# Kernel optimization log

Hardware: AMD Instinct MI355X
Metric: run time of the kernel (lower is better)

Reference implementation:

```python
import jax, jax.numpy as jnp
import numpy as np

B, W, N = 4, 8, 1024
F_IN, HID, OUT = 256, 256, 128


def setup_inputs() -> dict:
    key = jax.random.key(0)
    ks = jax.random.split(key, 8)
    X = jax.random.normal(ks[0], (B, W, N, F_IN), dtype=jnp.float32)
    adj = jax.random.uniform(ks[1], (B, W, N, N), dtype=jnp.float32)
    # Linear params, torch default init: U(-1/sqrt(fan_in), 1/sqrt(fan_in))
    def lin(k, fi, fo):
        k1, k2 = jax.random.split(k)
        bnd = 1.0 / np.sqrt(fi)
        Wm = jax.random.uniform(k1, (fi, fo), minval=-bnd, maxval=bnd, dtype=jnp.float32)
        bm = jax.random.uniform(k2, (fo,), minval=-bnd, maxval=bnd, dtype=jnp.float32)
        return Wm, bm
    W1, b1 = lin(ks[2], F_IN, HID)
    W2, b2 = lin(ks[3], HID, HID)
    W3, b3 = lin(ks[4], HID, OUT)
    return {"X": X, "adj": adj, "W1": W1, "b1": b1, "W2": W2, "b2": b2, "W3": W3, "b3": b3}


def _normalize(adj):
    # adj: [B, W, N, N]. adj_hat = adj + I; sym degree norm D^-1/2 A D^-1/2
    n = adj.shape[-1]
    adj_hat = adj + jnp.eye(n, dtype=adj.dtype)
    d = jnp.sum(adj_hat, axis=-1) ** (-0.5)            # [B, W, N]
    # diag(d) @ adj_hat @ diag(d) == row/col scaling (same math, no N^3 diag matmuls)
    return adj_hat * d[..., :, None] * d[..., None, :]


def reference(X, adj, W1, b1, W2, b2, W3, b3):
    adj_norm = _normalize(adj)                          # [B, W, N, N]
    h = X
    for Wm, bm in ((W1, b1), (W2, b2), (W3, b3)):
        h = jnp.einsum('bwnm,bwmf->bwnf', adj_norm, h)  # aggregate
        h = jax.nn.relu(jnp.einsum('bwnf,fo->bwno', h, Wm) + bm)
    return h                                            # [B, W, N, OUT]
```

## Files before the change

kernel.cpp:

```cpp
#include <hip/hip_runtime.h>
#include <hip/hip_bf16.h>
#include <cstdint>
#include <cstddef>

#define NN 1024
#define FF 256

typedef __attribute__((ext_vector_type(8))) short bf16x8;
typedef __attribute__((ext_vector_type(4))) float f32x4;

typedef __attribute__((address_space(1))) const void* gas_ptr;
typedef __attribute__((address_space(3))) void* las_ptr;

__device__ __forceinline__ short f2bf(float x) {
  unsigned int u = __float_as_uint(x);
  u = (u + 0x7fffu + ((u >> 16) & 1u)) >> 16;
  return (short)u;
}


__global__ __launch_bounds__(256)
void dinv_cast(const float* __restrict__ adj, float* __restrict__ dinv,
               short* __restrict__ Ahat) {
  __shared__ float wsum[64];
  int b = blockIdx.x;
  int bw = b >> 6, s = b & 63;
  int t = threadIdx.x;
  int wid = t >> 6, lane = t & 63;
  int row = lane & 15;
  int rloc = (s << 4) + row;
  int kg = (lane >> 4) & 3;
  const float* arow = adj + ((size_t)(bw << 10) + rloc) * NN;
  short* outb = Ahat + ((size_t)bw << 20) + ((size_t)s << 14) + (t << 3);
  float ssum = 0.f;
  #pragma unroll
  for (int it = 0; it < 8; it++) {
    int col = (it << 7) + (wid << 5) + (kg << 3);
    float4 a0 = *(const float4*)(arow + col);
    float4 a1 = *(const float4*)(arow + col + 4);
    float v[8] = {a0.x, a0.y, a0.z, a0.w, a1.x, a1.y, a1.z, a1.w};
    union { ushort o[8]; int4 q; } pk;
    #pragma unroll
    for (int j = 0; j < 8; j++) {
      v[j] += (rloc == col + j) ? 1.f : 0.f;
      ssum += v[j];
      pk.o[j] = (ushort)f2bf(v[j]);
    }
    *(int4*)(outb + (it << 11)) = pk.q;
  }
  ssum += __shfl_down(ssum, 32, 64);
  ssum += __shfl_down(ssum, 16, 64);
  if (lane < 16) wsum[(wid << 4) + lane] = ssum;
  __syncthreads();
  if (t < 16) {
    float tot = wsum[t] + wsum[16 + t] + wsum[32 + t] + wsum[48 + t];
    dinv[(bw << 10) + (s << 4) + t] = rsqrtf(tot);
  }
}

__global__ __launch_bounds__(256)
void transpose_x(const float* __restrict__ X, const float* __restrict__ dinv,
                 short* __restrict__ XT) {
  __shared__ short T[64][72];
  int bwo = blockIdx.z;
  int n0 = blockIdx.x << 6, f0 = blockIdx.y << 6;
  int t = threadIdx.x;
  {
    int n = t >> 2, fc = (t & 3) << 4;
    float dn = dinv[(bwo << 10) + n0 + n];
    const float* src = X + (((size_t)bwo * NN + n0 + n) * FF) + f0 + fc;
    #pragma unroll
    for (int i = 0; i < 4; i++) {
      float4 v = ((const float4*)src)[i];
      ushort4 p;
      p.x = (unsigned short)f2bf(v.x * dn); p.y = (unsigned short)f2bf(v.y * dn);
      p.z = (unsigned short)f2bf(v.z * dn); p.w = (unsigned short)f2bf(v.w * dn);
      *(ushort4*)&T[n][fc + (i << 2)] = p;
    }
  }
  __syncthreads();
  {
    int f = t >> 2, nc = (t & 3) << 4;
    int fg = f0 + f, ng = n0 + nc;
    short tmp[16];
    #pragma unroll
    for (int i = 0; i < 16; i++) tmp[i] = T[nc + i][f];
    size_t e0 = ((size_t)bwo << 18) + ((size_t)(fg >> 4) << 14) + ((ng >> 5) << 9)
              + (((ng & 31) >> 3) << 7) + ((fg & 15) << 3);
    *(int4*)(XT + e0)       = *(int4*)&tmp[0];
    *(int4*)(XT + e0 + 128) = *(int4*)&tmp[8];
  }
}

__global__ __launch_bounds__(256)
void transpose_w(const float* __restrict__ W, short* __restrict__ WT, int FO) {
  int idx = blockIdx.x * 256 + threadIdx.x;
  if (idx >= FO * 256) return;
  int fo = idx >> 8, fi = idx & 255;
  size_t e = (size_t)((fo >> 4) << 12) + ((fi >> 5) << 9)
           + (((fi & 31) >> 3) << 7) + ((fo & 15) << 3) + (fi & 7);
  WT[e] = f2bf(W[fi * FO + fo]);
}

template<int F_OUT, bool FINAL>
__global__ __launch_bounds__(512, 2)
void gcn_layer(const short* __restrict__ Ahat,
               const float* __restrict__ dinv,
               const short* __restrict__ Gin,
               const short* __restrict__ WT,
               const float* __restrict__ bias,
               short* __restrict__ Gout,
               float* __restrict__ Out) {
  __shared__ short lds[34816];

  int b = blockIdx.x;
  int x = b & 7, m = b >> 3;
  int bw = (x << 2) + (m >> 3);
  int rb = m & 7;
  int r0 = rb << 7;

  int tid = threadIdx.x;
  int wid = tid >> 6, lane = tid & 63;
  int l15 = lane & 15, l4 = lane >> 4;
  int wr = wid >> 2, wf = wid & 3;

  const short* Hb = Gin + ((size_t)bw << 18) + ((size_t)(wf << 2) << 14) + (lane << 3);
  const float* dvB = dinv + (bw << 10);

  auto stage = [&](int sel, int T) {
    const short* gb = Ahat + ((size_t)bw << 20) + ((size_t)(T << 1) << 9);
    short* dst = lds + (sel << 13);
    #pragma unroll
    for (int i = 0; i < 2; i++) {
      int slot = (i << 9) + tid;
      int s = slot >> 7, c = slot & 127;
      const short* g = gb + ((size_t)((rb << 3) + s) << 14) + (c << 3);
      __builtin_amdgcn_global_load_lds((gas_ptr)g, (las_ptr)(dst + (slot << 3)), 16, 0, 0);
    }
  };

  f32x4 acc[4][4];
  #pragma unroll
  for (int ah = 0; ah < 4; ah++)
    #pragma unroll
    for (int aa = 0; aa < 4; aa++) acc[ah][aa] = f32x4{0.f, 0.f, 0.f, 0.f};

  stage(0, 0);

  for (int t = 0; t < 16; ++t) {
    bf16x8 h[4][2];
    #pragma unroll
    for (int fh = 0; fh < 4; fh++) {
      h[fh][0] = *(const bf16x8*)(Hb + ((size_t)fh << 14) + ((size_t)(2 * t) << 9));
      h[fh][1] = *(const bf16x8*)(Hb + ((size_t)fh << 14) + ((size_t)(2 * t + 1) << 9));
    }
    asm volatile("s_waitcnt vmcnt(8)" ::: "memory");
    __builtin_amdgcn_sched_barrier(0);
    __builtin_amdgcn_s_barrier();
    __builtin_amdgcn_sched_barrier(0);
    if (t < 15) stage((t + 1) & 1, t + 1);
    const short* ab = lds + ((t & 1) << 13);
    bf16x8 a[4][2];
    #pragma unroll
    for (int aa = 0; aa < 4; aa++) {
      int sa = (wr << 2) + aa;
      a[aa][0] = *(const bf16x8*)(ab + (sa << 10) + (lane << 3));
      a[aa][1] = *(const bf16x8*)(ab + (sa << 10) + 512 + (lane << 3));
    }
    __builtin_amdgcn_s_setprio(1);
    #pragma unroll
    for (int kt = 0; kt < 2; kt++)
      #pragma unroll
      for (int ah = 0; ah < 4; ah++)
        #pragma unroll
        for (int aa = 0; aa < 4; aa++)
          acc[ah][aa] = __builtin_amdgcn_mfma_f32_16x16x32_bf16(
              h[ah][kt], a[aa][kt], acc[ah][aa], 0, 0, 0);
    __builtin_amdgcn_s_setprio(0);
  }

  __builtin_amdgcn_sched_barrier(0);
  __builtin_amdgcn_s_barrier();
  __builtin_amdgcn_sched_barrier(0);

  float dsc[4];
  #pragma unroll
  for (int aa = 0; aa < 4; aa++) dsc[aa] = dvB[r0 + (wr << 6) + (aa << 4) + l15];
  #pragma unroll
  for (int ah = 0; ah < 4; ah++)
    #pragma unroll
    for (int aa = 0; aa < 4; aa++) {
      int r = (wr << 6) + (aa << 4) + l15;
      int fB = ((wf << 6) + (ah << 4) + (l4 << 2)) << 1;
      int off = (r * 544 + (fB ^ ((r & 7) << 4))) >> 1;
      ushort4 p;
      p.x = (unsigned short)f2bf(acc[ah][aa][0] * dsc[aa]);
      p.y = (unsigned short)f2bf(acc[ah][aa][1] * dsc[aa]);
      p.z = (unsigned short)f2bf(acc[ah][aa][2] * dsc[aa]);
      p.w = (unsigned short)f2bf(acc[ah][aa][3] * dsc[aa]);
      *(ushort4*)(lds + off) = p;
    }
  asm volatile("s_waitcnt lgkmcnt(0)" ::: "memory");
  __builtin_amdgcn_sched_barrier(0);
  __builtin_amdgcn_s_barrier();
  __builtin_amdgcn_sched_barrier(0);

  constexpr int NFO = F_OUT / 64;
  const short* Wbase = WT + (size_t)(wf * NFO) * 4096 + (lane << 3);
  f32x4 acc2[4][NFO];
  #pragma unroll
  for (int am = 0; am < 4; am++)
    #pragma unroll
    for (int nf = 0; nf < NFO; nf++) acc2[am][nf] = f32x4{0.f, 0.f, 0.f, 0.f};

  #pragma unroll
  for (int kt = 0; kt < 8; kt++) {
    bf16x8 af[4];
    #pragma unroll
    for (int am = 0; am < 4; am++) {
      int r = (wr << 6) + (am << 4) + l15;
      int fB = (kt << 6) + (l4 << 4);
      af[am] = *(const bf16x8*)(lds + ((r * 544 + (fB ^ ((r & 7) << 4))) >> 1));
    }
    #pragma unroll
    for (int nf = 0; nf < NFO; nf++) {
      bf16x8 wv = *(const bf16x8*)(Wbase + (size_t)nf * 4096 + (kt << 9));
      #pragma unroll
      for (int am = 0; am < 4; am++)
        acc2[am][nf] = __builtin_amdgcn_mfma_f32_16x16x32_bf16(af[am], wv, acc2[am][nf], 0, 0, 0);
    }
  }

  #pragma unroll
  for (int am = 0; am < 4; am++) {
    int nodeLoc = (wr << 6) + (am << 4) + (l4 << 2);
    float4 dn4 = *(const float4*)(dvB + r0 + nodeLoc);
    float dn[4] = {dn4.x, dn4.y, dn4.z, dn4.w};
    #pragma unroll
    for (int nf = 0; nf < NFO; nf++) {
      int fo = wf * (F_OUT / 4) + (nf << 4) + l15;
      float bb = bias[fo];
      float v[4];
      #pragma unroll
      for (int j = 0; j < 4; j++) v[j] = fmaxf(acc2[am][nf][j] + bb, 0.f);
      if (!FINAL) {
        ushort4 p;
        p.x = (unsigned short)f2bf(v[0] * dn[0]);
        p.y = (unsigned short)f2bf(v[1] * dn[1]);
        p.z = (unsigned short)f2bf(v[2] * dn[2]);
        p.w = (unsigned short)f2bf(v[3] * dn[3]);
        size_t e = (size_t)bw * (F_OUT * 1024) + ((size_t)(fo >> 4) << 14)
                 + ((size_t)((rb << 2) + (wr << 1) + (am >> 1)) << 9)
                 + ((size_t)(((am & 1) << 1) + (l4 >> 1)) << 7)
                 + ((fo & 15) << 3) + ((l4 & 1) << 2);
        *(ushort4*)(Gout + e) = p;
      } else {
        float* ob = Out + ((size_t)(bw << 10) + r0 + nodeLoc) * F_OUT + fo;
        ob[0]         = v[0];
        ob[F_OUT]     = v[1];
        ob[2 * F_OUT] = v[2];
        ob[3 * F_OUT] = v[3];
      }
    }
  }
}

extern "C" void kernel_launch(void* const* d_in, const int* in_sizes, int n_in,
                              void* d_out, int out_size, void* d_ws, size_t ws_size,
                              hipStream_t stream) {
  const float* X   = (const float*)d_in[0];
  const float* adj = (const float*)d_in[1];
  const float* W1  = (const float*)d_in[2];
  const float* b1  = (const float*)d_in[3];
  const float* W2  = (const float*)d_in[4];
  const float* b2  = (const float*)d_in[5];
  const float* W3  = (const float*)d_in[6];
  const float* b3  = (const float*)d_in[7];
  float* out = (float*)d_out;

  char* ws = (char*)d_ws;
  float* dinv = (float*)ws;
  short* WT1  = (short*)(ws + 131072);
  short* WT2  = (short*)(ws + 262144);
  short* WT3  = (short*)(ws + 393216);
  short* bufA = (short*)(ws + 458752);
  short* bufB = (short*)(ws + 458752 + 16777216);
  short* Ahat = (short*)(ws + 458752 + 2 * 16777216);

  dinv_cast<<<2048, 256, 0, stream>>>(adj, dinv, Ahat);
  transpose_x<<<dim3(16, 4, 32), 256, 0, stream>>>(X, dinv, bufA);
  transpose_w<<<256, 256, 0, stream>>>(W1, WT1, 256);
  transpose_w<<<256, 256, 0, stream>>>(W2, WT2, 256);
  transpose_w<<<128, 256, 0, stream>>>(W3, WT3, 128);

  gcn_layer<256, false><<<256, 512, 0, stream>>>(Ahat, dinv, bufA, WT1, b1, bufB, nullptr);
  gcn_layer<256, false><<<256, 512, 0, stream>>>(Ahat, dinv, bufB, WT2, b2, bufA, nullptr);
  gcn_layer<128, true ><<<256, 512, 0, stream>>>(Ahat, dinv, bufA, WT3, b3, nullptr, out);
}
```

Before: 148.5 us.

## Stage H tiles through LDS with async loads and merge weight transposes

The aggregation loop now loads the H (feature) tiles into a larger double-buffered LDS region with global_load_lds, next to the adjacency tiles, instead of loading them per wave straight into registers. This is meant to cut redundant global traffic and make the prefetch fully asynchronous. The three weight-transpose launches are merged into one kernel to save launch overhead. In exchange, LDS per block grows to 96KB and the launch bounds drop the 2-blocks hint, which may lower occupancy, and each iteration now ends with a full vmcnt(0) wait and barrier.

```diff
diff --git a/kernel.cpp b/kernel.cpp
--- a/kernel.cpp
+++ b/kernel.cpp
@@ -93,17 +93,24 @@
 }
 
 __global__ __launch_bounds__(256)
-void transpose_w(const float* __restrict__ W, short* __restrict__ WT, int FO) {
+void transpose_w3(const float* __restrict__ W1, const float* __restrict__ W2,
+                  const float* __restrict__ W3,
+                  short* __restrict__ T1, short* __restrict__ T2,
+                  short* __restrict__ T3) {
   int idx = blockIdx.x * 256 + threadIdx.x;
-  if (idx >= FO * 256) return;
-  int fo = idx >> 8, fi = idx & 255;
+  const float* W; short* T; int FO; int loc;
+  if (idx < 65536)       { W = W1; T = T1; FO = 256; loc = idx; }
+  else if (idx < 131072) { W = W2; T = T2; FO = 256; loc = idx - 65536; }
+  else                   { W = W3; T = T3; FO = 128; loc = idx - 131072; }
+  int fo = loc >> 8, fi = loc & 255;
+  if (fo >= FO) return;
   size_t e = (size_t)((fo >> 4) << 12) + ((fi >> 5) << 9)
            + (((fi & 31) >> 3) << 7) + ((fo & 15) << 3) + (fi & 7);
-  WT[e] = f2bf(W[fi * FO + fo]);
+  T[e] = f2bf(W[fi * FO + fo]);
 }
 
 template<int F_OUT, bool FINAL>
-__global__ __launch_bounds__(512, 2)
+__global__ __launch_bounds__(512)
 void gcn_layer(const short* __restrict__ Ahat,
                const float* __restrict__ dinv,
                const short* __restrict__ Gin,
@@ -111,7 +118,7 @@
                const float* __restrict__ bias,
                short* __restrict__ Gout,
                float* __restrict__ Out) {
-  __shared__ short lds[34816];
+  __shared__ __align__(16) short lds[49152];
 
   int b = blockIdx.x;
   int x = b & 7, m = b >> 3;
@@ -124,18 +131,26 @@
   int l15 = lane & 15, l4 = lane >> 4;
   int wr = wid >> 2, wf = wid & 3;
 
-  const short* Hb = Gin + ((size_t)bw << 18) + ((size_t)(wf << 2) << 14) + (lane << 3);
   const float* dvB = dinv + (bw << 10);
-
-  auto stage = [&](int sel, int T) {
-    const short* gb = Ahat + ((size_t)bw << 20) + ((size_t)(T << 1) << 9);
-    short* dst = lds + (sel << 13);
+  const short* Abase = Ahat + ((size_t)bw << 20) + ((size_t)(rb << 3) << 14);
+  const short* Hbase = Gin  + ((size_t)bw << 18);
+
+  auto stage = [&](int sel, int t) {
+    char* base = (char*)lds + sel * 49152;
+    int kb = t << 1;
     #pragma unroll
     for (int i = 0; i < 2; i++) {
       int slot = (i << 9) + tid;
-      int s = slot >> 7, c = slot & 127;
-      const short* g = gb + ((size_t)((rb << 3) + s) << 14) + (c << 3);
-      __builtin_amdgcn_global_load_lds((gas_ptr)g, (las_ptr)(dst + (slot << 3)), 16, 0, 0);
+      int c = slot >> 6, o = slot & 63;
+      const short* g = Abase + ((size_t)(c >> 1) << 14) + ((size_t)(kb + (c & 1)) << 9) + (o << 3);
+      __builtin_amdgcn_global_load_lds((gas_ptr)g, (las_ptr)(base + (slot << 4)), 16, 0, 0);
+    }
+    #pragma unroll
+    for (int i = 0; i < 4; i++) {
+      int slot = (i << 9) + tid;
+      int c = slot >> 6, o = slot & 63;
+      const short* g = Hbase + ((size_t)(c >> 1) << 14) + ((size_t)(kb + (c & 1)) << 9) + (o << 3);
+      __builtin_amdgcn_global_load_lds((gas_ptr)g, (las_ptr)(base + 16384 + (slot << 4)), 16, 0, 0);
     }
   };
 
@@ -146,26 +161,24 @@
     for (int aa = 0; aa < 4; aa++) acc[ah][aa] = f32x4{0.f, 0.f, 0.f, 0.f};
 
   stage(0, 0);
+  asm volatile("s_waitcnt vmcnt(0)" ::: "memory");
+  __builtin_amdgcn_s_barrier();
 
   for (int t = 0; t < 16; ++t) {
-    bf16x8 h[4][2];
-    #pragma unroll
-    for (int fh = 0; fh < 4; fh++) {
-      h[fh][0] = *(const bf16x8*)(Hb + ((size_t)fh << 14) + ((size_t)(2 * t) << 9));
-      h[fh][1] = *(const bf16x8*)(Hb + ((size_t)fh << 14) + ((size_t)(2 * t + 1) << 9));
-    }
-    asm volatile("s_waitcnt vmcnt(8)" ::: "memory");
-    __builtin_amdgcn_sched_barrier(0);
-    __builtin_amdgcn_s_barrier();
-    __builtin_amdgcn_sched_barrier(0);
     if (t < 15) stage((t + 1) & 1, t + 1);
-    const short* ab = lds + ((t & 1) << 13);
-    bf16x8 a[4][2];
+    const char* base = (const char*)lds + (t & 1) * 49152;
+    bf16x8 a[4][2], h[4][2];
     #pragma unroll
     for (int aa = 0; aa < 4; aa++) {
-      int sa = (wr << 2) + aa;
-      a[aa][0] = *(const bf16x8*)(ab + (sa << 10) + (lane << 3));
-      a[aa][1] = *(const bf16x8*)(ab + (sa << 10) + 512 + (lane << 3));
+      int c = ((wr << 2) + aa) << 1;
+      a[aa][0] = *(const bf16x8*)(base + (c << 10) + (lane << 4));
+      a[aa][1] = *(const bf16x8*)(base + ((c + 1) << 10) + (lane << 4));
+    }
+    #pragma unroll
+    for (int ah = 0; ah < 4; ah++) {
+      int c = ((wf << 2) + ah) << 1;
+      h[ah][0] = *(const bf16x8*)(base + 16384 + (c << 10) + (lane << 4));
+      h[ah][1] = *(const bf16x8*)(base + 16384 + ((c + 1) << 10) + (lane << 4));
     }
     __builtin_amdgcn_s_setprio(1);
     #pragma unroll
@@ -177,12 +190,12 @@
           acc[ah][aa] = __builtin_amdgcn_mfma_f32_16x16x32_bf16(
               h[ah][kt], a[aa][kt], acc[ah][aa], 0, 0, 0);
     __builtin_amdgcn_s_setprio(0);
-  }
-
-  __builtin_amdgcn_sched_barrier(0);
-  __builtin_amdgcn_s_barrier();
-  __builtin_amdgcn_sched_barrier(0);
-
+    asm volatile("s_waitcnt vmcnt(0)" ::: "memory");
+    __builtin_amdgcn_sched_barrier(0);
+    __builtin_amdgcn_s_barrier();
+  }
+
+  short* aggL = lds;
   float dsc[4];
   #pragma unroll
   for (int aa = 0; aa < 4; aa++) dsc[aa] = dvB[r0 + (wr << 6) + (aa << 4) + l15];
@@ -198,12 +211,9 @@
       p.y = (unsigned short)f2bf(acc[ah][aa][1] * dsc[aa]);
       p.z = (unsigned short)f2bf(acc[ah][aa][2] * dsc[aa]);
       p.w = (unsigned short)f2bf(acc[ah][aa][3] * dsc[aa]);
-      *(ushort4*)(lds + off) = p;
-    }
-  asm volatile("s_waitcnt lgkmcnt(0)" ::: "memory");
-  __builtin_amdgcn_sched_barrier(0);
-  __builtin_amdgcn_s_barrier();
-  __builtin_amdgcn_sched_barrier(0);
+      *(ushort4*)(aggL + off) = p;
+    }
+  __syncthreads();
 
   constexpr int NFO = F_OUT / 64;
   const short* Wbase = WT + (size_t)(wf * NFO) * 4096 + (lane << 3);
@@ -220,7 +230,7 @@
     for (int am = 0; am < 4; am++) {
       int r = (wr << 6) + (am << 4) + l15;
       int fB = (kt << 6) + (l4 << 4);
-      af[am] = *(const bf16x8*)(lds + ((r * 544 + (fB ^ ((r & 7) << 4))) >> 1));
+      af[am] = *(const bf16x8*)(aggL + ((r * 544 + (fB ^ ((r & 7) << 4))) >> 1));
     }
     #pragma unroll
     for (int nf = 0; nf < NFO; nf++) {
@@ -288,10 +298,8 @@
   short* Ahat = (short*)(ws + 458752 + 2 * 16777216);
 
   dinv_cast<<<2048, 256, 0, stream>>>(adj, dinv, Ahat);
+  transpose_w3<<<640, 256, 0, stream>>>(W1, W2, W3, WT1, WT2, WT3);
   transpose_x<<<dim3(16, 4, 32), 256, 0, stream>>>(X, dinv, bufA);
-  transpose_w<<<256, 256, 0, stream>>>(W1, WT1, 256);
-  transpose_w<<<256, 256, 0, stream>>>(W2, WT2, 256);
-  transpose_w<<<128, 256, 0, stream>>>(W3, WT3, 128);
 
   gcn_layer<256, false><<<256, 512, 0, stream>>>(Ahat, dinv, bufA, WT1, b1, bufB, nullptr);
   gcn_layer<256, false><<<256, 512, 0, stream>>>(Ahat, dinv, bufB, WT2, b2, bufA, nullptr);
```

After: 133.4 us. -10.1%, faster.
